# Kernel optimization log

Measured on AMD Instinct MI355X. Metric: run time of the kernel, lower is better.

Reference implementation:

```python
import jax, jax.numpy as jnp
import numpy as np

N, D_IN, H, C, K = 16384, 2048, 4096, 256, 256


def setup_inputs() -> dict:
    key = jax.random.key(0)
    ks = jax.random.split(key, 13)

    def lin(kw, kb, fan_in, fan_out):
        # torch Linear default init: U(-1/sqrt(fan_in), 1/sqrt(fan_in)); stored as [in, out]
        bound = 1.0 / np.sqrt(fan_in)
        W = jax.random.uniform(kw, (fan_in, fan_out), jnp.float32, -bound, bound)
        b = jax.random.uniform(kb, (fan_out,), jnp.float32, -bound, bound)
        return W, b

    W_e1, b_e1 = lin(ks[0], ks[1], D_IN, H)
    W_e2, b_e2 = lin(ks[2], ks[3], H, C)
    W_d1, b_d1 = lin(ks[4], ks[5], C, H)
    W_d2, b_d2 = lin(ks[6], ks[7], H, D_IN)
    # codebooks init U(-1/K, 1/K) per the torch code
    cb1 = jax.random.uniform(ks[8], (K, C), jnp.float32, -1.0 / K, 1.0 / K)
    cb2 = jax.random.uniform(ks[9], (K, C), jnp.float32, -1.0 / K, 1.0 / K)
    cb3 = jax.random.uniform(ks[10], (K, C), jnp.float32, -1.0 / K, 1.0 / K)
    x = jax.random.normal(ks[11], (N, D_IN), jnp.float32)
    return {"x": x, "W_e1": W_e1, "b_e1": b_e1, "W_e2": W_e2, "b_e2": b_e2,
            "cb1": cb1, "cb2": cb2, "cb3": cb3,
            "W_d1": W_d1, "b_d1": b_d1, "W_d2": W_d2, "b_d2": b_d2}


def _vq_stage(z, cb):
    # dist[n,k] = sum_c (cb[k,c] - z[n,c])^2 = ||z||^2 - 2 z.cb^T + ||cb||^2
    # (same math as the torch N x K x C broadcast, expressed as a GEMM)
    d = (jnp.sum(z * z, axis=1, keepdims=True)
         - 2.0 * (z @ cb.T)
         + jnp.sum(cb * cb, axis=1))            # [N, K]
    nearest = jnp.argmin(d, axis=1)             # [N]
    zq = cb[nearest]                            # gather [N, C]
    return nearest, zq


def reference(x, W_e1, b_e1, W_e2, b_e2, cb1, cb2, cb3, W_d1, b_d1, W_d2, b_d2):
    ze_1 = jax.nn.relu(x @ W_e1 + b_e1) @ W_e2 + b_e2     # [N, C]
    nearest_1, zq_1 = _vq_stage(ze_1, cb1)
    ze_2 = ze_1 - zq_1
    nearest_2, zq_2 = _vq_stage(ze_2, cb2)
    ze_3 = ze_2 - zq_2
    nearest_3, zq_3 = _vq_stage(ze_3, cb3)
    # straight-through estimator
    decoder_input = ze_1 + jax.lax.stop_gradient(zq_1 + zq_2 + zq_3 - ze_1)
    x_hat = jax.nn.sigmoid(decoder_input @ W_d1 + b_d1) @ W_d2 + b_d2
    return (x_hat, ze_1, ze_2, ze_3, zq_1, zq_2, zq_3, nearest_1, nearest_2, nearest_3)
```

## Files before the change

### kernel.cpp

```cpp
#include <hip/hip_runtime.h>
#include <cstddef>


#define NN 16384
#define DIN 2048
#define HH 4096
#define CC 256
#define QRED ((size_t)4096 * 256)

typedef unsigned short ushortT;
typedef __attribute__((ext_vector_type(8))) short bf16x8;
typedef __attribute__((ext_vector_type(4))) float f32x4;

__device__ __forceinline__ ushortT f2b(float v) {
    unsigned int u = __float_as_uint(v);
    return (ushortT)((u + 0x7fffu + ((u >> 16) & 1u)) >> 16);
}
__device__ __forceinline__ float b2f(ushortT s) {
    return __uint_as_float(((unsigned int)s) << 16);
}
__device__ __forceinline__ void split3(float v, ushortT& h, ushortT& m, ushortT& l) {
    h = f2b(v);
    float r1 = v - b2f(h);
    m = f2b(r1);
    l = f2b(r1 - b2f(m));
}

__device__ __forceinline__ void gld16(const void* g, void* l) {
    __builtin_amdgcn_global_load_lds(
        (const __attribute__((address_space(1))) unsigned int*)g,
        (__attribute__((address_space(3))) unsigned int*)l,
        16, 0, 0);
}

template<int NP>
__launch_bounds__(256)
__global__ void tsplit(const float* __restrict__ W,
                       ushortT* __restrict__ T0,
                       ushortT* __restrict__ T1,
                       ushortT* __restrict__ T2,
                       int K, int N)
{
    __shared__ float tile[32][33];
    const int k0 = blockIdx.y * 32, n0 = blockIdx.x * 32;
    const int c = threadIdx.x & 31, r = threadIdx.x >> 5;
    #pragma unroll
    for (int i = 0; i < 4; ++i)
        tile[r + 8*i][c] = W[(size_t)(k0 + r + 8*i) * N + n0 + c];
    __syncthreads();
    #pragma unroll
    for (int i = 0; i < 4; ++i) {
        const int nl = r + 8*i, kl = c;
        float v = tile[kl][nl];
        size_t o = (size_t)(n0 + nl) * K + k0 + kl;
        ushortT h = f2b(v);
        T0[o] = h;
        if (NP > 1) {
            float r1 = v - b2f(h);
            ushortT m = f2b(r1);
            T1[o] = m;
            T2[o] = f2b(r1 - b2f(m));
        }
    }
}

__launch_bounds__(256)
__global__ void split_src(const float* __restrict__ X,
                          ushortT* __restrict__ P0, ushortT* __restrict__ P1,
                          ushortT* __restrict__ P2, size_t n4)
{
    for (size_t i = (size_t)blockIdx.x * 256 + threadIdx.x; i < n4;
         i += (size_t)gridDim.x * 256) {
        float4 v = *(const float4*)(X + i * 4);
        ushort4 hv, mv, lv;
        split3(v.x, ((ushortT*)&hv)[0], ((ushortT*)&mv)[0], ((ushortT*)&lv)[0]);
        split3(v.y, ((ushortT*)&hv)[1], ((ushortT*)&mv)[1], ((ushortT*)&lv)[1]);
        split3(v.z, ((ushortT*)&hv)[2], ((ushortT*)&mv)[2], ((ushortT*)&lv)[2]);
        split3(v.w, ((ushortT*)&hv)[3], ((ushortT*)&mv)[3], ((ushortT*)&lv)[3]);
        *(ushort4*)(P0 + i * 4) = hv;
        *(ushort4*)(P1 + i * 4) = mv;
        *(ushort4*)(P2 + i * 4) = lv;
    }
}

template<int NSEG, int KSH, int NTC, int EPI, int OM>
__launch_bounds__(512, 2)
__global__ void gemm256(const ushortT* __restrict__ Ab, size_t aPl,
                        const ushortT* __restrict__ Bb, size_t bPl,
                        const float* __restrict__ bias,
                        float* __restrict__ Cf,
                        ushortT* __restrict__ Ob, size_t oPl,
                        int N, int K)
{
    __shared__ ushortT sh[65536];

    const int t    = threadIdx.x;
    const int lane = t & 63;
    const int wid  = t >> 6;
    const int l15  = lane & 15;
    const int l4   = lane >> 4;
    const int bm   = blockIdx.y * 256;
    const int bn   = blockIdx.x * 256;
    const int wm   = (wid >> 2) * 128;
    const int wn   = (wid & 3) * 64;
    const int t0   = (OM == 3) ? blockIdx.z * NTC : 0;

    constexpr unsigned PA_PACK = 0x210100u;
    constexpr unsigned PB_PACK = 0x012010u;

    const int trow = t >> 3;
    const unsigned tcol = (unsigned)(((t & 7) ^ (trow & 7)) * 8);
    unsigned gA[4], gB[4];
    #pragma unroll
    for (int i = 0; i < 4; ++i) {
        gA[i] = (unsigned)(bm + i * 64 + trow) * (unsigned)K + tcol;
        gB[i] = (unsigned)(bn + i * 64 + trow) * (unsigned)K + tcol;
    }
    const int ldsT = t * 8;

    auto stage = [&](int buf, int gtt) {
        const int seg = (NSEG > 1) ? (gtt >> KSH) : 0;
        const unsigned kin = ((unsigned)(gtt & ((1 << KSH) - 1))) << 6;
        const unsigned pa = (NSEG > 1) ? ((PA_PACK >> (seg * 4)) & 15u) : 0u;
        const unsigned pb = (NSEG > 1) ? ((PB_PACK >> (seg * 4)) & 15u) : 0u;
        const ushortT* Abase = Ab + (size_t)pa * aPl + kin;
        const ushortT* Bbase = Bb + (size_t)pb * bPl + kin;
        ushortT* lb = sh + buf * 32768;
        #pragma unroll
        for (int i = 0; i < 4; ++i)
            gld16(Abase + gA[i], lb + i * 4096 + ldsT);
        #pragma unroll
        for (int i = 0; i < 4; ++i)
            gld16(Bbase + gB[i], lb + 16384 + i * 4096 + ldsT);
    };

    f32x4 acc[8][4] = {};

    stage(0, t0);
    stage(1, t0 + 1);

    #pragma unroll 1
    for (int tt = 0; tt < NTC; ++tt) {
        const int buf = tt & 1;
        if (tt + 1 < NTC) { asm volatile("s_waitcnt vmcnt(8)" ::: "memory"); }
        else              { asm volatile("s_waitcnt vmcnt(0)" ::: "memory"); }
        __builtin_amdgcn_sched_barrier(0);
        __builtin_amdgcn_s_barrier();
        __builtin_amdgcn_sched_barrier(0);

        const ushortT* As = sh + buf * 32768;
        const ushortT* Bs = As + 16384;
        __builtin_amdgcn_s_setprio(1);
        #pragma unroll
        for (int kk = 0; kk < 2; ++kk) {
            bf16x8 bfr[4];
            #pragma unroll
            for (int ni = 0; ni < 4; ++ni) {
                const int rb = wn + ni * 16 + l15;
                bfr[ni] = *(const bf16x8*)&Bs[rb * 64 + (((kk << 2) | l4) ^ (rb & 7)) * 8];
            }
            #pragma unroll
            for (int mi = 0; mi < 8; ++mi) {
                const int ra = wm + mi * 16 + l15;
                bf16x8 af = *(const bf16x8*)&As[ra * 64 + (((kk << 2) | l4) ^ (ra & 7)) * 8];
                #pragma unroll
                for (int ni = 0; ni < 4; ++ni)
                    acc[mi][ni] = __builtin_amdgcn_mfma_f32_16x16x32_bf16(
                        af, bfr[ni], acc[mi][ni], 0, 0, 0);
            }
        }
        __builtin_amdgcn_s_setprio(0);
        __builtin_amdgcn_sched_barrier(0);
        asm volatile("" ::: "memory");
        __builtin_amdgcn_s_barrier();
        __builtin_amdgcn_sched_barrier(0);

        if (tt + 2 < NTC) stage(buf, t0 + tt + 2);
    }

    #pragma unroll
    for (int ni = 0; ni < 4; ++ni) {
        const int gcol = bn + wn + ni * 16 + l15;
        float bvv = 0.0f;
        if (OM != 3) bvv = bias[gcol];
        #pragma unroll
        for (int mi = 0; mi < 8; ++mi) {
            #pragma unroll
            for (int r = 0; r < 4; ++r) {
                const int grow = bm + wm + mi * 16 + l4 * 4 + r;
                const size_t o = (size_t)grow * N + gcol;
                if (OM == 3) {
                    Cf[(size_t)blockIdx.z * oPl + o] = acc[mi][ni][r];
                } else {
                    float v = acc[mi][ni][r] + bvv;
                    if (EPI == 1) v = fmaxf(v, 0.0f);
                    if (EPI == 2) v = 1.0f / (1.0f + expf(-v));
                    if (OM == 0) {
                        Cf[o] = v;
                    } else if (OM == 2) {
                        Ob[o] = f2b(v);
                    } else {
                        ushortT hh, mm, ll;
                        split3(v, hh, mm, ll);
                        Ob[o] = hh; Ob[oPl + o] = mm; Ob[2 * oPl + o] = ll;
                    }
                }
            }
        }
    }
}

__launch_bounds__(256)
__global__ void reduce_z(const float* __restrict__ part,
                         const float* __restrict__ bias,
                         float* __restrict__ outp, int n4)
{
    const int i = blockIdx.x * 256 + threadIdx.x;
    if (i >= n4) return;
    float4 s = *(const float4*)(part + (size_t)i * 4);
    #pragma unroll
    for (int z = 1; z < 12; ++z) {
        float4 p = *(const float4*)(part + (size_t)z * (QRED) + (size_t)i * 4);
        s.x = __fadd_rn(s.x, p.x); s.y = __fadd_rn(s.y, p.y);
        s.z = __fadd_rn(s.z, p.z); s.w = __fadd_rn(s.w, p.w);
    }
    const int c4 = (i * 4) & 255;
    float4 b = *(const float4*)(bias + c4);
    s.x = __fadd_rn(s.x, b.x); s.y = __fadd_rn(s.y, b.y);
    s.z = __fadd_rn(s.z, b.z); s.w = __fadd_rn(s.w, b.w);
    *(float4*)(outp + (size_t)i * 4) = s;
}

__launch_bounds__(256)
__global__ void vq_kernel(const float* __restrict__ ze1,
                          const float* __restrict__ cb1,
                          const float* __restrict__ cb2,
                          const float* __restrict__ cb3,
                          float* __restrict__ out_ze2, float* __restrict__ out_ze3,
                          float* __restrict__ out_zq1, float* __restrict__ out_zq2,
                          float* __restrict__ out_zq3,
                          float* __restrict__ out_n1,  float* __restrict__ out_n2,
                          float* __restrict__ out_n3,
                          ushortT* __restrict__ dec_p)
{
    __shared__ float Zs[16][260];
    __shared__ float Ds[16][260];
    __shared__ float DecS[16][260];
    __shared__ float Srow[16];
    __shared__ int   Kmin[16];

    const int t    = threadIdx.x;
    const int row0 = blockIdx.x * 16;

    for (int i = t; i < 16*64; i += 256) {
        int r = i >> 6, c4 = (i & 63) << 2;
        float4 v = *(const float4*)(ze1 + (size_t)(row0 + r) * 256 + c4);
        *(float4*)&Zs[r][c4] = v;
        float4 z = {0.f,0.f,0.f,0.f};
        *(float4*)&DecS[r][c4] = z;
    }
    __syncthreads();

    const float* cbs[3] = {cb1, cb2, cb3};
    float* zqs[3] = {out_zq1, out_zq2, out_zq3};
    float* nss[3] = {out_n1, out_n2, out_n3};

    for (int s = 0; s < 3; ++s) {
        const float* cb = cbs[s];
        if (t < 16) {
            float ssum = 0.f;
            for (int c = 0; c < 256; ++c) ssum = fmaf(Zs[t][c], Zs[t][c], ssum);
            Srow[t] = ssum;
        }
        __syncthreads();
        {
            float accr[16];
            #pragma unroll
            for (int r = 0; r < 16; ++r) accr[r] = 0.f;
            float c2 = 0.f;
            const float* cbrow = cb + (size_t)t * 256;
            for (int c4 = 0; c4 < 256; c4 += 4) {
                float4 cv = *(const float4*)(cbrow + c4);
                c2 = fmaf(cv.x,cv.x,fmaf(cv.y,cv.y,fmaf(cv.z,cv.z,fmaf(cv.w,cv.w,c2))));
                #pragma unroll
                for (int r = 0; r < 16; ++r) {
                    float4 zv = *(const float4*)&Zs[r][c4];
                    accr[r] = fmaf(zv.x,cv.x,fmaf(zv.y,cv.y,
                              fmaf(zv.z,cv.z,fmaf(zv.w,cv.w,accr[r]))));
                }
            }
            #pragma unroll
            for (int r = 0; r < 16; ++r) {
                float g2 = __fmul_rn(2.0f, accr[r]);
                float t1 = __fsub_rn(Srow[r], g2);
                Ds[r][t]  = __fadd_rn(t1, c2);
            }
        }
        __syncthreads();
        if (t < 16) {
            float best = Ds[t][0];
            int bk = 0;
            for (int k = 1; k < 256; ++k) {
                float v = Ds[t][k];
                if (v < best) { best = v; bk = k; }
            }
            Kmin[t] = bk;
            nss[s][row0 + t] = (float)bk;
        }
        __syncthreads();
        for (int i = t; i < 16*64; i += 256) {
            int r = i >> 6, c4 = (i & 63) << 2;
            const float* q = cb + (size_t)Kmin[r] * 256 + c4;
            float4 qv = *(const float4*)q;
            *(float4*)&zqs[s][(size_t)(row0 + r) * 256 + c4] = qv;
            float4 dv = *(float4*)&DecS[r][c4];
            dv.x = __fadd_rn(dv.x, qv.x); dv.y = __fadd_rn(dv.y, qv.y);
            dv.z = __fadd_rn(dv.z, qv.z); dv.w = __fadd_rn(dv.w, qv.w);
            *(float4*)&DecS[r][c4] = dv;
            if (s < 2) {
                float4 zv = *(float4*)&Zs[r][c4];
                zv.x = __fsub_rn(zv.x, qv.x); zv.y = __fsub_rn(zv.y, qv.y);
                zv.z = __fsub_rn(zv.z, qv.z); zv.w = __fsub_rn(zv.w, qv.w);
                *(float4*)&Zs[r][c4] = zv;
                float* oz = (s == 0) ? out_ze2 : out_ze3;
                *(float4*)&oz[(size_t)(row0 + r) * 256 + c4] = zv;
            }
        }
        __syncthreads();
    }

    for (int i = t; i < 16*64; i += 256) {
        int r = i >> 6, c4 = (i & 63) << 2;
        float4 z1 = *(const float4*)(ze1 + (size_t)(row0 + r) * 256 + c4);
        float4 dv = *(float4*)&DecS[r][c4];
        float4 o;
        o.x = __fadd_rn(z1.x, __fsub_rn(dv.x, z1.x));
        o.y = __fadd_rn(z1.y, __fsub_rn(dv.y, z1.y));
        o.z = __fadd_rn(z1.z, __fsub_rn(dv.z, z1.z));
        o.w = __fadd_rn(z1.w, __fsub_rn(dv.w, z1.w));
        ushort4 ov;
        ((ushortT*)&ov)[0] = f2b(o.x);
        ((ushortT*)&ov)[1] = f2b(o.y);
        ((ushortT*)&ov)[2] = f2b(o.z);
        ((ushortT*)&ov)[3] = f2b(o.w);
        *(ushort4*)(dec_p + (size_t)(row0 + r) * 256 + c4) = ov;
    }
}

extern "C" void kernel_launch(void* const* d_in, const int* in_sizes, int n_in,
                              void* d_out, int out_size, void* d_ws, size_t ws_size,
                              hipStream_t stream)
{
    const float* x   = (const float*)d_in[0];
    const float* We1 = (const float*)d_in[1];
    const float* be1 = (const float*)d_in[2];
    const float* We2 = (const float*)d_in[3];
    const float* be2 = (const float*)d_in[4];
    const float* cb1 = (const float*)d_in[5];
    const float* cb2 = (const float*)d_in[6];
    const float* cb3 = (const float*)d_in[7];
    const float* Wd1 = (const float*)d_in[8];
    const float* bd1 = (const float*)d_in[9];
    const float* Wd2 = (const float*)d_in[10];
    const float* bd2 = (const float*)d_in[11];

    float* out   = (float*)d_out;
    float* x_hat = out;
    float* ze1   = out + 33554432;
    float* ze2   = out + 37748736;
    float* ze3   = out + 41943040;
    float* zq1   = out + 46137344;
    float* zq2   = out + 50331648;
    float* zq3   = out + 54525952;
    float* n1    = out + 58720256;
    float* n2    = out + 58736640;
    float* n3    = out + 58753024;

    const int    QR   = 4096;
    const size_t szXq = (size_t)QR * DIN;
    const size_t szHq = (size_t)QR * HH;
    const size_t szW1 = (size_t)HH * DIN;
    const size_t szW2 = (size_t)CC * HH;

    ushortT* xq   = (ushortT*)d_ws;
    ushortT* hq   = xq + 3 * szXq;
    ushortT* We1t = hq + 3 * szHq;
    ushortT* We2t = We1t + 3 * szW1;
    ushortT* Wd1t = We2t + 3 * szW2;
    ushortT* Wd2t = Wd1t + szW2;
    ushortT* decp = Wd2t + szW1;
    float*   zpart = (float*)(decp + (size_t)NN * CC);
    ushortT* h2p  = xq;

    dim3 blk(256), blk5(512);

    tsplit<3><<<dim3(HH/32, DIN/32), blk, 0, stream>>>(We1, We1t, We1t+szW1, We1t+2*szW1, DIN, HH);
    tsplit<3><<<dim3(CC/32, HH/32),  blk, 0, stream>>>(We2, We2t, We2t+szW2, We2t+2*szW2, HH, CC);
    tsplit<1><<<dim3(HH/32, CC/32),  blk, 0, stream>>>(Wd1, Wd1t, nullptr, nullptr, CC, HH);
    tsplit<1><<<dim3(DIN/32, HH/32), blk, 0, stream>>>(Wd2, Wd2t, nullptr, nullptr, HH, DIN);

    for (int q = 0; q < 4; ++q) {
        split_src<<<dim3(2048), blk, 0, stream>>>(x + (size_t)q * szXq,
                                                  xq, xq + szXq, xq + 2*szXq, szXq / 4);
        gemm256<6,5,192,1,1><<<dim3(HH/256, QR/256), blk5, 0, stream>>>(
            xq, szXq, We1t, szW1, be1, nullptr, hq, szHq, HH, DIN);
        gemm256<6,6,32,0,3><<<dim3(CC/256, QR/256, 12), blk5, 0, stream>>>(
            hq, szHq, We2t, szW2, nullptr, zpart, nullptr, QRED, CC, HH);
        reduce_z<<<dim3(QR*CC/4/256), blk, 0, stream>>>(
            zpart, be2, ze1 + (size_t)q * QR * CC, QR*CC/4);
    }

    vq_kernel<<<dim3(NN/16), blk, 0, stream>>>(ze1, cb1, cb2, cb3,
                                               ze2, ze3, zq1, zq2, zq3,
                                               n1, n2, n3, decp);

    gemm256<1,2,4,2,2><<<dim3(HH/256, NN/256), blk5, 0, stream>>>(
        decp, 0, Wd1t, 0, bd1, nullptr, h2p, 0, HH, CC);
    gemm256<1,6,64,0,0><<<dim3(DIN/256, NN/256), blk5, 0, stream>>>(
        h2p, 0, Wd2t, 0, bd2, x_hat, nullptr, 0, DIN, HH);
}
```

Before: 2.451 ms.

## Split GEMM k-tile into four MFMA phases with half-tile interleaved prefetch

The GEMM main loop is restructured into four sub-phases per k-tile, each covering half of M and half of K. The next tile's global-to-LDS load is split into two halves, issued between phases. Finer vmcnt waits let compute start before the whole tile arrives, and the load order is arranged so each phase only needs the data already waited on. Prefetch depth drops from two tiles to one, and more barriers are added per tile. Separately, the encoder second GEMM's split-K count doubles from 12 to 24 for more parallelism, at the cost of more partial-sum traffic in reduce_z and a larger zpart buffer.

```diff
diff --git a/kernel.cpp b/kernel.cpp
--- a/kernel.cpp
+++ b/kernel.cpp
@@ -7,6 +7,7 @@
 #define HH 4096
 #define CC 256
 #define QRED ((size_t)4096 * 256)
+#define NZ 24
 
 typedef unsigned short ushortT;
 typedef __attribute__((ext_vector_type(8))) short bf16x8;
@@ -118,7 +119,7 @@
     }
     const int ldsT = t * 8;
 
-    auto stage = [&](int buf, int gtt) {
+    auto stageH = [&](int buf, int gtt, int half) {
         const int seg = (NSEG > 1) ? (gtt >> KSH) : 0;
         const unsigned kin = ((unsigned)(gtt & ((1 << KSH) - 1))) << 6;
         const unsigned pa = (NSEG > 1) ? ((PA_PACK >> (seg * 4)) & 15u) : 0u;
@@ -126,56 +127,124 @@
         const ushortT* Abase = Ab + (size_t)pa * aPl + kin;
         const ushortT* Bbase = Bb + (size_t)pb * bPl + kin;
         ushortT* lb = sh + buf * 32768;
-        #pragma unroll
-        for (int i = 0; i < 4; ++i)
-            gld16(Abase + gA[i], lb + i * 4096 + ldsT);
-        #pragma unroll
-        for (int i = 0; i < 4; ++i)
-            gld16(Bbase + gB[i], lb + 16384 + i * 4096 + ldsT);
+        if (half == 0) {
+            gld16(Abase + gA[0], lb + 0 * 4096 + ldsT);
+            gld16(Abase + gA[2], lb + 2 * 4096 + ldsT);
+            gld16(Bbase + gB[0], lb + 16384 + 0 * 4096 + ldsT);
+            gld16(Bbase + gB[1], lb + 16384 + 1 * 4096 + ldsT);
+        } else {
+            gld16(Bbase + gB[2], lb + 16384 + 2 * 4096 + ldsT);
+            gld16(Bbase + gB[3], lb + 16384 + 3 * 4096 + ldsT);
+            gld16(Abase + gA[1], lb + 1 * 4096 + ldsT);
+            gld16(Abase + gA[3], lb + 3 * 4096 + ldsT);
+        }
     };
 
     f32x4 acc[8][4] = {};
 
-    stage(0, t0);
-    stage(1, t0 + 1);
+    stageH(0, t0, 0);
+    stageH(0, t0, 1);
 
     #pragma unroll 1
     for (int tt = 0; tt < NTC; ++tt) {
         const int buf = tt & 1;
-        if (tt + 1 < NTC) { asm volatile("s_waitcnt vmcnt(8)" ::: "memory"); }
-        else              { asm volatile("s_waitcnt vmcnt(0)" ::: "memory"); }
-        __builtin_amdgcn_sched_barrier(0);
-        __builtin_amdgcn_s_barrier();
-        __builtin_amdgcn_sched_barrier(0);
-
         const ushortT* As = sh + buf * 32768;
         const ushortT* Bs = As + 16384;
+        const bool notlast = (tt + 1 < NTC);
+        bf16x8 a_[4], b_[4];
+
+        asm volatile("s_waitcnt vmcnt(2)" ::: "memory");
+        __builtin_amdgcn_sched_barrier(0);
+        __builtin_amdgcn_s_barrier();
+        __builtin_amdgcn_sched_barrier(0);
+        #pragma unroll
+        for (int ni = 0; ni < 4; ++ni) {
+            const int rb = wn + ni * 16 + l15;
+            b_[ni] = *(const bf16x8*)&Bs[rb * 64 + (l4 ^ (rb & 7)) * 8];
+        }
+        #pragma unroll
+        for (int mi = 0; mi < 4; ++mi) {
+            const int ra = wm + mi * 16 + l15;
+            a_[mi] = *(const bf16x8*)&As[ra * 64 + (l4 ^ (ra & 7)) * 8];
+        }
+        if (notlast) stageH(buf ^ 1, t0 + tt + 1, 0);
+        asm volatile("s_waitcnt lgkmcnt(0)" ::: "memory");
+        __builtin_amdgcn_sched_barrier(0);
         __builtin_amdgcn_s_setprio(1);
         #pragma unroll
-        for (int kk = 0; kk < 2; ++kk) {
-            bf16x8 bfr[4];
-            #pragma unroll
-            for (int ni = 0; ni < 4; ++ni) {
-                const int rb = wn + ni * 16 + l15;
-                bfr[ni] = *(const bf16x8*)&Bs[rb * 64 + (((kk << 2) | l4) ^ (rb & 7)) * 8];
-            }
-            #pragma unroll
-            for (int mi = 0; mi < 8; ++mi) {
-                const int ra = wm + mi * 16 + l15;
-                bf16x8 af = *(const bf16x8*)&As[ra * 64 + (((kk << 2) | l4) ^ (ra & 7)) * 8];
-                #pragma unroll
-                for (int ni = 0; ni < 4; ++ni)
-                    acc[mi][ni] = __builtin_amdgcn_mfma_f32_16x16x32_bf16(
-                        af, bfr[ni], acc[mi][ni], 0, 0, 0);
-            }
-        }
+        for (int mi = 0; mi < 4; ++mi)
+            #pragma unroll
+            for (int ni = 0; ni < 4; ++ni)
+                acc[mi][ni] = __builtin_amdgcn_mfma_f32_16x16x32_bf16(
+                    a_[mi], b_[ni], acc[mi][ni], 0, 0, 0);
         __builtin_amdgcn_s_setprio(0);
         __builtin_amdgcn_sched_barrier(0);
-        asm volatile("" ::: "memory");
+
+        if (notlast) { asm volatile("s_waitcnt vmcnt(4)" ::: "memory"); }
+        else         { asm volatile("s_waitcnt vmcnt(0)" ::: "memory"); }
+        __builtin_amdgcn_sched_barrier(0);
         __builtin_amdgcn_s_barrier();
         __builtin_amdgcn_sched_barrier(0);
-
-        if (tt + 2 < NTC) stage(buf, t0 + tt + 2);
+        #pragma unroll
+        for (int mi = 0; mi < 4; ++mi) {
+            const int ra = wm + (mi + 4) * 16 + l15;
+            a_[mi] = *(const bf16x8*)&As[ra * 64 + (l4 ^ (ra & 7)) * 8];
+        }
+        if (notlast) stageH(buf ^ 1, t0 + tt + 1, 1);
+        asm volatile("s_waitcnt lgkmcnt(0)" ::: "memory");
+        __builtin_amdgcn_sched_barrier(0);
+        __builtin_amdgcn_s_setprio(1);
+        #pragma unroll
+        for (int mi = 0; mi < 4; ++mi)
+            #pragma unroll
+            for (int ni = 0; ni < 4; ++ni)
+                acc[mi + 4][ni] = __builtin_amdgcn_mfma_f32_16x16x32_bf16(
+                    a_[mi], b_[ni], acc[mi + 4][ni], 0, 0, 0);
+        __builtin_amdgcn_s_setprio(0);
+        __builtin_amdgcn_sched_barrier(0);
+
+        __builtin_amdgcn_s_barrier();
+        __builtin_amdgcn_sched_barrier(0);
+        #pragma unroll
+        for (int ni = 0; ni < 4; ++ni) {
+            const int rb = wn + ni * 16 + l15;
+            b_[ni] = *(const bf16x8*)&Bs[rb * 64 + ((4 | l4) ^ (rb & 7)) * 8];
+        }
+        #pragma unroll
+        for (int mi = 0; mi < 4; ++mi) {
+            const int ra = wm + mi * 16 + l15;
+            a_[mi] = *(const bf16x8*)&As[ra * 64 + ((4 | l4) ^ (ra & 7)) * 8];
+        }
+        asm volatile("s_waitcnt lgkmcnt(0)" ::: "memory");
+        __builtin_amdgcn_sched_barrier(0);
+        __builtin_amdgcn_s_setprio(1);
+        #pragma unroll
+        for (int mi = 0; mi < 4; ++mi)
+            #pragma unroll
+            for (int ni = 0; ni < 4; ++ni)
+                acc[mi][ni] = __builtin_amdgcn_mfma_f32_16x16x32_bf16(
+                    a_[mi], b_[ni], acc[mi][ni], 0, 0, 0);
+        __builtin_amdgcn_s_setprio(0);
+        __builtin_amdgcn_sched_barrier(0);
+
+        __builtin_amdgcn_s_barrier();
+        __builtin_amdgcn_sched_barrier(0);
+        #pragma unroll
+        for (int mi = 0; mi < 4; ++mi) {
+            const int ra = wm + (mi + 4) * 16 + l15;
+            a_[mi] = *(const bf16x8*)&As[ra * 64 + ((4 | l4) ^ (ra & 7)) * 8];
+        }
+        asm volatile("s_waitcnt lgkmcnt(0)" ::: "memory");
+        __builtin_amdgcn_sched_barrier(0);
+        __builtin_amdgcn_s_setprio(1);
+        #pragma unroll
+        for (int mi = 0; mi < 4; ++mi)
+            #pragma unroll
+            for (int ni = 0; ni < 4; ++ni)
+                acc[mi + 4][ni] = __builtin_amdgcn_mfma_f32_16x16x32_bf16(
+                    a_[mi], b_[ni], acc[mi + 4][ni], 0, 0, 0);
+        __builtin_amdgcn_s_setprio(0);
+        __builtin_amdgcn_sched_barrier(0);
     }
 
     #pragma unroll
@@ -219,7 +288,7 @@
     if (i >= n4) return;
     float4 s = *(const float4*)(part + (size_t)i * 4);
     #pragma unroll
-    for (int z = 1; z < 12; ++z) {
+    for (int z = 1; z < NZ; ++z) {
         float4 p = *(const float4*)(part + (size_t)z * (QRED) + (size_t)i * 4);
         s.x = __fadd_rn(s.x, p.x); s.y = __fadd_rn(s.y, p.y);
         s.z = __fadd_rn(s.z, p.z); s.w = __fadd_rn(s.w, p.w);
@@ -404,7 +473,7 @@
                                                   xq, xq + szXq, xq + 2*szXq, szXq / 4);
         gemm256<6,5,192,1,1><<<dim3(HH/256, QR/256), blk5, 0, stream>>>(
             xq, szXq, We1t, szW1, be1, nullptr, hq, szHq, HH, DIN);
-        gemm256<6,6,32,0,3><<<dim3(CC/256, QR/256, 12), blk5, 0, stream>>>(
+        gemm256<6,6,16,0,3><<<dim3(CC/256, QR/256, NZ), blk5, 0, stream>>>(
             hq, szHq, We2t, szW2, nullptr, zpart, nullptr, QRED, CC, HH);
         reduce_z<<<dim3(QR*CC/4/256), blk, 0, stream>>>(
             zpart, be2, ze1 + (size_t)q * QR * CC, QR*CC/4);
```

Result: no change. 2.434 ms (-0.7%).

## Replace 256x256 GEMM tile with 128x256 tile, K=32 steps and single-stage prefetch

Applied to the files above, without the earlier changes.

Rewrites the GEMM kernel to use a 128x256 block tile with 4 waves, a K-step of 32 instead of 64, and smaller LDS buffers. Fragments are loaded into registers before the next tile's global loads are issued, so only one barrier is needed per iteration. The split-K partition for the second encoder GEMM grows from 12 to 24 to keep enough blocks in flight. The intent is better occupancy and less LDS per block. In exchange there are twice as many loop iterations with a full vmcnt(0) wait each time, less reuse per tile, and more partial-sum traffic through reduce_z.

```diff
diff --git a/kernel.cpp b/kernel.cpp
--- a/kernel.cpp
+++ b/kernel.cpp
@@ -7,6 +7,7 @@
 #define HH 4096
 #define CC 256
 #define QRED ((size_t)4096 * 256)
+#define NZ 24
 
 typedef unsigned short ushortT;
 typedef __attribute__((ext_vector_type(8))) short bf16x8;
@@ -84,98 +85,101 @@
 }
 
 template<int NSEG, int KSH, int NTC, int EPI, int OM>
-__launch_bounds__(512, 2)
-__global__ void gemm256(const ushortT* __restrict__ Ab, size_t aPl,
+__launch_bounds__(256, 2)
+__global__ void gemm128(const ushortT* __restrict__ Ab, size_t aPl,
                         const ushortT* __restrict__ Bb, size_t bPl,
                         const float* __restrict__ bias,
                         float* __restrict__ Cf,
                         ushortT* __restrict__ Ob, size_t oPl,
                         int N, int K)
 {
-    __shared__ ushortT sh[65536];
+    __shared__ ushortT sh[24576];
 
     const int t    = threadIdx.x;
     const int lane = t & 63;
     const int wid  = t >> 6;
     const int l15  = lane & 15;
     const int l4   = lane >> 4;
-    const int bm   = blockIdx.y * 256;
+    const int bm   = blockIdx.y * 128;
     const int bn   = blockIdx.x * 256;
-    const int wm   = (wid >> 2) * 128;
-    const int wn   = (wid & 3) * 64;
+    const int wn   = wid * 64;
     const int t0   = (OM == 3) ? blockIdx.z * NTC : 0;
 
     constexpr unsigned PA_PACK = 0x210100u;
     constexpr unsigned PB_PACK = 0x012010u;
 
-    const int trow = t >> 3;
-    const unsigned tcol = (unsigned)(((t & 7) ^ (trow & 7)) * 8);
-    unsigned gA[4], gB[4];
+    unsigned gA[2], gB[4];
+    #pragma unroll
+    for (int i = 0; i < 2; ++i) {
+        const int c = i * 256 + t;
+        const int row = c >> 2, slot = c & 3;
+        const int colsw = (slot ^ ((row >> 1) & 3)) * 8;
+        gA[i] = (unsigned)(bm + row) * (unsigned)K + colsw;
+    }
     #pragma unroll
     for (int i = 0; i < 4; ++i) {
-        gA[i] = (unsigned)(bm + i * 64 + trow) * (unsigned)K + tcol;
-        gB[i] = (unsigned)(bn + i * 64 + trow) * (unsigned)K + tcol;
-    }
-    const int ldsT = t * 8;
+        const int c = i * 256 + t;
+        const int row = c >> 2, slot = c & 3;
+        const int colsw = (slot ^ ((row >> 1) & 3)) * 8;
+        gB[i] = (unsigned)(bn + row) * (unsigned)K + colsw;
+    }
 
     auto stage = [&](int buf, int gtt) {
         const int seg = (NSEG > 1) ? (gtt >> KSH) : 0;
-        const unsigned kin = ((unsigned)(gtt & ((1 << KSH) - 1))) << 6;
+        const unsigned kin = ((unsigned)(gtt & ((1 << KSH) - 1))) << 5;
         const unsigned pa = (NSEG > 1) ? ((PA_PACK >> (seg * 4)) & 15u) : 0u;
         const unsigned pb = (NSEG > 1) ? ((PB_PACK >> (seg * 4)) & 15u) : 0u;
         const ushortT* Abase = Ab + (size_t)pa * aPl + kin;
         const ushortT* Bbase = Bb + (size_t)pb * bPl + kin;
-        ushortT* lb = sh + buf * 32768;
+        ushortT* lb = sh + buf * 12288;
+        #pragma unroll
+        for (int i = 0; i < 2; ++i)
+            gld16(Abase + gA[i], lb + (i * 256 + t) * 8);
         #pragma unroll
         for (int i = 0; i < 4; ++i)
-            gld16(Abase + gA[i], lb + i * 4096 + ldsT);
-        #pragma unroll
-        for (int i = 0; i < 4; ++i)
-            gld16(Bbase + gB[i], lb + 16384 + i * 4096 + ldsT);
+            gld16(Bbase + gB[i], lb + 4096 + (i * 256 + t) * 8);
     };
 
     f32x4 acc[8][4] = {};
 
     stage(0, t0);
-    stage(1, t0 + 1);
 
     #pragma unroll 1
     for (int tt = 0; tt < NTC; ++tt) {
         const int buf = tt & 1;
-        if (tt + 1 < NTC) { asm volatile("s_waitcnt vmcnt(8)" ::: "memory"); }
-        else              { asm volatile("s_waitcnt vmcnt(0)" ::: "memory"); }
+        const ushortT* As = sh + buf * 12288;
+        const ushortT* Bs = As + 4096;
+        const bool notlast = (tt + 1 < NTC);
+        bf16x8 a_[8], b_[4];
+
+        asm volatile("s_waitcnt vmcnt(0)" ::: "memory");
         __builtin_amdgcn_sched_barrier(0);
         __builtin_amdgcn_s_barrier();
         __builtin_amdgcn_sched_barrier(0);
 
-        const ushortT* As = sh + buf * 32768;
-        const ushortT* Bs = As + 16384;
+        #pragma unroll
+        for (int ni = 0; ni < 4; ++ni) {
+            const int rb = wn + ni * 16 + l15;
+            b_[ni] = *(const bf16x8*)&Bs[rb * 32 + (l4 ^ ((rb >> 1) & 3)) * 8];
+        }
+        #pragma unroll
+        for (int mi = 0; mi < 8; ++mi) {
+            const int ra = mi * 16 + l15;
+            a_[mi] = *(const bf16x8*)&As[ra * 32 + (l4 ^ ((ra >> 1) & 3)) * 8];
+        }
+        if (notlast) stage(buf ^ 1, t0 + tt + 1);
+        __builtin_amdgcn_sched_barrier(0);
+        asm volatile("s_waitcnt lgkmcnt(0)" ::: "memory");
+        __builtin_amdgcn_sched_barrier(0);
         __builtin_amdgcn_s_setprio(1);
         #pragma unroll
-        for (int kk = 0; kk < 2; ++kk) {
-            bf16x8 bfr[4];
+        for (int mi = 0; mi < 8; ++mi)
             #pragma unroll
-            for (int ni = 0; ni < 4; ++ni) {
-                const int rb = wn + ni * 16 + l15;
-                bfr[ni] = *(const bf16x8*)&Bs[rb * 64 + (((kk << 2) | l4) ^ (rb & 7)) * 8];
-            }
-            #pragma unroll
-            for (int mi = 0; mi < 8; ++mi) {
-                const int ra = wm + mi * 16 + l15;
-                bf16x8 af = *(const bf16x8*)&As[ra * 64 + (((kk << 2) | l4) ^ (ra & 7)) * 8];
-                #pragma unroll
-                for (int ni = 0; ni < 4; ++ni)
-                    acc[mi][ni] = __builtin_amdgcn_mfma_f32_16x16x32_bf16(
-                        af, bfr[ni], acc[mi][ni], 0, 0, 0);
-            }
-        }
+            for (int ni = 0; ni < 4; ++ni)
+                acc[mi][ni] = __builtin_amdgcn_mfma_f32_16x16x32_bf16(
+                    a_[mi], b_[ni], acc[mi][ni], 0, 0, 0);
         __builtin_amdgcn_s_setprio(0);
         __builtin_amdgcn_sched_barrier(0);
-        asm volatile("" ::: "memory");
-        __builtin_amdgcn_s_barrier();
-        __builtin_amdgcn_sched_barrier(0);
-
-        if (tt + 2 < NTC) stage(buf, t0 + tt + 2);
     }
 
     #pragma unroll
@@ -187,7 +191,7 @@
         for (int mi = 0; mi < 8; ++mi) {
             #pragma unroll
             for (int r = 0; r < 4; ++r) {
-                const int grow = bm + wm + mi * 16 + l4 * 4 + r;
+                const int grow = bm + mi * 16 + l4 * 4 + r;
                 const size_t o = (size_t)grow * N + gcol;
                 if (OM == 3) {
                     Cf[(size_t)blockIdx.z * oPl + o] = acc[mi][ni][r];
@@ -219,7 +223,7 @@
     if (i >= n4) return;
     float4 s = *(const float4*)(part + (size_t)i * 4);
     #pragma unroll
-    for (int z = 1; z < 12; ++z) {
+    for (int z = 1; z < NZ; ++z) {
         float4 p = *(const float4*)(part + (size_t)z * (QRED) + (size_t)i * 4);
         s.x = __fadd_rn(s.x, p.x); s.y = __fadd_rn(s.y, p.y);
         s.z = __fadd_rn(s.z, p.z); s.w = __fadd_rn(s.w, p.w);
@@ -392,7 +396,7 @@
     float*   zpart = (float*)(decp + (size_t)NN * CC);
     ushortT* h2p  = xq;
 
-    dim3 blk(256), blk5(512);
+    dim3 blk(256);
 
     tsplit<3><<<dim3(HH/32, DIN/32), blk, 0, stream>>>(We1, We1t, We1t+szW1, We1t+2*szW1, DIN, HH);
     tsplit<3><<<dim3(CC/32, HH/32),  blk, 0, stream>>>(We2, We2t, We2t+szW2, We2t+2*szW2, HH, CC);
@@ -402,9 +406,9 @@
     for (int q = 0; q < 4; ++q) {
         split_src<<<dim3(2048), blk, 0, stream>>>(x + (size_t)q * szXq,
                                                   xq, xq + szXq, xq + 2*szXq, szXq / 4);
-        gemm256<6,5,192,1,1><<<dim3(HH/256, QR/256), blk5, 0, stream>>>(
+        gemm128<6,6,384,1,1><<<dim3(HH/256, QR/128), blk, 0, stream>>>(
             xq, szXq, We1t, szW1, be1, nullptr, hq, szHq, HH, DIN);
-        gemm256<6,6,32,0,3><<<dim3(CC/256, QR/256, 12), blk5, 0, stream>>>(
+        gemm128<6,7,32,0,3><<<dim3(CC/256, QR/128, NZ), blk, 0, stream>>>(
             hq, szHq, We2t, szW2, nullptr, zpart, nullptr, QRED, CC, HH);
         reduce_z<<<dim3(QR*CC/4/256), blk, 0, stream>>>(
             zpart, be2, ze1 + (size_t)q * QR * CC, QR*CC/4);
@@ -414,8 +418,8 @@
                                                ze2, ze3, zq1, zq2, zq3,
                                                n1, n2, n3, decp);
 
-    gemm256<1,2,4,2,2><<<dim3(HH/256, NN/256), blk5, 0, stream>>>(
+    gemm128<1,3,8,2,2><<<dim3(HH/256, NN/128), blk, 0, stream>>>(
         decp, 0, Wd1t, 0, bd1, nullptr, h2p, 0, HH, CC);
-    gemm256<1,6,64,0,0><<<dim3(DIN/256, NN/256), blk5, 0, stream>>>(
+    gemm128<1,7,128,0,0><<<dim3(DIN/256, NN/128), blk, 0, stream>>>(
         h2p, 0, Wd2t, 0, bd2, x_hat, nullptr, 0, DIN, HH);
 }
```

Result: slower. 2.692 ms (+9.9%).
